# Kernel optimization log

Hardware: AMD Instinct MI355X
Metric: run time of the kernel (lower is better)

The kernel has to match this reference:

```python
import jax, jax.numpy as jnp
import numpy as np

B, S, D, H = 2, 2048, 1024, 16  # batch, seq_len, model dim, heads


def setup_inputs() -> dict:
    key = jax.random.key(0)
    ks = jax.random.split(key, 5)
    return {
        "x": jax.random.normal(ks[0], (B, S, D), jnp.float32),
        "idx": jax.random.randint(ks[1], (B,), 0, S),
        "weight": jnp.float32(0.5),
        "attn_forcing": 1,  # static python flag
        "w_qkv": jax.random.normal(ks[2], (D, 3 * D), jnp.float32) * 0.02,
        "b_qkv": jnp.zeros((3 * D,), jnp.float32),
        "w_proj": jax.random.normal(ks[3], (D, D), jnp.float32) * 0.02,
        "b_proj": jnp.zeros((D,), jnp.float32),
    }


def reference(x, idx, weight, attn_forcing, w_qkv, b_qkv, w_proj, b_proj):
    Bx, Sx, Dm = x.shape
    dh = Dm // H
    # qkv projection (Conv1D: x @ w + b)
    qkv = x @ w_qkv + b_qkv  # [B,S,3D]
    q, k, v = jnp.split(qkv, 3, axis=-1)
    q = q.reshape(Bx, Sx, H, dh).transpose(0, 2, 1, 3)  # [B,H,S,dh]
    k = k.reshape(Bx, Sx, H, dh).transpose(0, 2, 1, 3)
    v = v.reshape(Bx, Sx, H, dh).transpose(0, 2, 1, 3)
    alen = jnp.arange(Sx)
    mask = (alen[None, :] <= alen[:, None]).astype(x.dtype)  # [S,S] causal
    w = jnp.einsum('bhqd,bhkd->bhqk', q, k) / jnp.asarray(np.sqrt(dh), x.dtype)
    w = w * mask + jnp.asarray(-1e9, x.dtype) * (1 - mask)
    w = jax.nn.softmax(w, axis=-1)
    if attn_forcing:
        # post-softmax forcing reweight: positions >= idx scaled by weight, then renorm
        a = jnp.where(alen[None, :] >= idx[:, None], weight, jnp.asarray(1.0, x.dtype))  # [B,S]
        w = w * a[:, None, None, :]
        w = w / jnp.sum(w, axis=-1, keepdims=True)
    out = jnp.einsum('bhqk,bhkd->bhqd', w, v)  # [B,H,S,dh]
    out = out.transpose(0, 2, 1, 3).reshape(Bx, Sx, Dm)  # merge heads
    return out @ w_proj + b_proj
```

## Files before the change

### kernel.cpp

```cpp
#include <hip/hip_runtime.h>


typedef __attribute__((ext_vector_type(8))) short short8;
typedef __attribute__((ext_vector_type(4))) float f32x4;

#define MFMA_B16(a, b, c) __builtin_amdgcn_mfma_f32_16x16x32_bf16(a, b, c, 0, 0, 0)

#if __has_builtin(__builtin_amdgcn_exp2f)
#define EXP2(x) __builtin_amdgcn_exp2f(x)
#else
#define EXP2(x) exp2f(x)
#endif

static __device__ __forceinline__ unsigned short f2bf(float f) {
    union { float f; unsigned int u; } v;
    v.f = f;
    unsigned int r = (v.u + 0x7fffu + ((v.u >> 16) & 1u)) >> 16;
    return (unsigned short)r;
}

static __device__ __forceinline__ unsigned int pk_bf16(float a, float b) {
#if __has_builtin(__builtin_amdgcn_cvt_pk_bf16_f32)
    typedef __bf16 bf2 __attribute__((ext_vector_type(2)));
    union { bf2 v; unsigned int u; } c;
    c.v = __builtin_amdgcn_cvt_pk_bf16_f32(a, b);
    return c.u;
#else
    return (unsigned int)f2bf(a) | ((unsigned int)f2bf(b) << 16);
#endif
}

static __device__ __forceinline__ void gl_lds16(const void* g, void* l) {
    __builtin_amdgcn_global_load_lds(
        (const __attribute__((address_space(1))) unsigned int*)g,
        (__attribute__((address_space(3))) unsigned int*)l, 16, 0, 0);
}

__global__ __launch_bounds__(256) void prep_kernel(const float4* __restrict__ x,
                                                   ushort4* __restrict__ xb,
                                                   const float* __restrict__ wqkv,
                                                   unsigned short* __restrict__ wqkvT,
                                                   const float* __restrict__ wproj,
                                                   unsigned short* __restrict__ wprojT) {
    const int bid = blockIdx.x;
    if (bid < 4096) {
        int i = bid * 256 + threadIdx.x;
        float4 v = x[i];
        ushort4 o;
        o.x = f2bf(v.x); o.y = f2bf(v.y); o.z = f2bf(v.z); o.w = f2bf(v.w);
        xb[i] = o;
        return;
    }
    __shared__ float t[32][33];
    const float* in;
    unsigned short* out;
    int R, C, bx, by;
    if (bid < 4096 + 3072) {
        int g = bid - 4096;
        in = wqkv; out = wqkvT; R = 1024; C = 3072;
        bx = g % 96; by = g / 96;
    } else {
        int g = bid - 7168;
        in = wproj; out = wprojT; R = 1024; C = 1024;
        bx = g & 31; by = g >> 5;
    }
    const int c0 = bx * 32, r0 = by * 32;
    const int xx = threadIdx.x & 31, yy0 = threadIdx.x >> 5;
    #pragma unroll
    for (int yy = yy0; yy < 32; yy += 8)
        t[yy][xx] = in[(size_t)(r0 + yy) * C + (c0 + xx)];
    __syncthreads();
    #pragma unroll
    for (int yy = yy0; yy < 32; yy += 8)
        out[(size_t)(c0 + yy) * R + (r0 + xx)] = f2bf(t[xx][yy]);
}

__global__ __launch_bounds__(256) void gemm_qkv_kernel(const unsigned short* __restrict__ A,
                                                       const unsigned short* __restrict__ Bt,
                                                       const float* __restrict__ bias,
                                                       unsigned short* __restrict__ q,
                                                       unsigned short* __restrict__ k,
                                                       unsigned short* __restrict__ vT) {
    __shared__ unsigned short As[128 * 64];
    __shared__ unsigned short Bs[128 * 64];
    const int tid = threadIdx.x;
    const int lane = tid & 63, wave = tid >> 6;
    const int l15 = lane & 15, quad = lane >> 4;
    const int wm = wave >> 1, wn = wave & 1;
    const int row0 = blockIdx.y * 128, col0 = blockIdx.x * 128;
    const int K = 1024;
    const bool isV = (blockIdx.x >= 16);

    int srow[4], scol[4], sdst[4];
    #pragma unroll
    for (int h = 0; h < 4; ++h) {
        int D = h * 256 + wave * 64 + lane;
        srow[h] = D >> 3;
        scol[h] = ((D & 7) ^ (srow[h] & 7)) * 8;
        sdst[h] = (h * 256 + wave * 64) * 8;
    }

    f32x4 acc[4][4] = {};

    for (int kt = 0; kt < K; kt += 64) {
        #pragma unroll
        for (int h = 0; h < 4; ++h) {
            gl_lds16(&A[(size_t)(row0 + srow[h]) * K + kt + scol[h]], &As[sdst[h]]);
            gl_lds16(&Bt[(size_t)(col0 + srow[h]) * K + kt + scol[h]], &Bs[sdst[h]]);
        }
        __syncthreads();
        #pragma unroll
        for (int kk = 0; kk < 2; ++kk) {
            short8 af[4], bf[4];
            #pragma unroll
            for (int i = 0; i < 4; ++i) {
                int r = wm * 64 + i * 16 + l15;
                af[i] = *(const short8*)&As[r * 64 + (((kk * 4 + quad) ^ (r & 7)) * 8)];
            }
            #pragma unroll
            for (int j = 0; j < 4; ++j) {
                int r = wn * 64 + j * 16 + l15;
                bf[j] = *(const short8*)&Bs[r * 64 + (((kk * 4 + quad) ^ (r & 7)) * 8)];
            }
            if (isV) {
                #pragma unroll
                for (int i = 0; i < 4; ++i)
                    #pragma unroll
                    for (int j = 0; j < 4; ++j)
                        acc[i][j] = MFMA_B16(af[i], bf[j], acc[i][j]);
            } else {
                #pragma unroll
                for (int i = 0; i < 4; ++i)
                    #pragma unroll
                    for (int j = 0; j < 4; ++j)
                        acc[i][j] = MFMA_B16(bf[j], af[i], acc[i][j]);
            }
        }
        __syncthreads();
    }

    const int b = row0 >> 11;
    const int s0 = row0 & 2047;
    const float* bb = bias + col0 + wn * 64;

    if (!isV) {
        const int which = blockIdx.x >> 3;
        unsigned short* dst = which ? k : q;
        const float scale = which ? 1.0f : 0.1803368867f;
        const int hh = ((blockIdx.x & 7) << 1) + wn;
        #pragma unroll
        for (int i = 0; i < 4; ++i) {
            const int s = s0 + wm * 64 + i * 16 + l15;
            unsigned short* drow = dst + ((size_t)((b * 16 + hh) * 2048 + s)) * 64;
            #pragma unroll
            for (int j = 0; j < 4; ++j) {
                float4 b4 = ((const float4*)bb)[j * 4 + quad];
                uint2 pv;
                pv.x = pk_bf16((acc[i][j][0] + b4.x) * scale, (acc[i][j][1] + b4.y) * scale);
                pv.y = pk_bf16((acc[i][j][2] + b4.z) * scale, (acc[i][j][3] + b4.w) * scale);
                *(uint2*)&drow[j * 16 + quad * 4] = pv;
            }
        }
    } else {
        const int hh = ((blockIdx.x - 16) << 1) + wn;
        #pragma unroll
        for (int j = 0; j < 4; ++j) {
            const int d = j * 16 + l15;
            const float bv = bb[d];
            unsigned short* drow = vT + ((size_t)((b * 16 + hh) * 64 + d)) * 2048 + s0;
            #pragma unroll
            for (int i = 0; i < 4; ++i) {
                uint2 pv;
                pv.x = pk_bf16(acc[i][j][0] + bv, acc[i][j][1] + bv);
                pv.y = pk_bf16(acc[i][j][2] + bv, acc[i][j][3] + bv);
                *(uint2*)&drow[wm * 64 + i * 16 + quad * 4] = pv;
            }
        }
    }
}

__global__ __launch_bounds__(256) void gemm_proj_kernel(const unsigned short* __restrict__ A,
                                                        const unsigned short* __restrict__ Bt,
                                                        const float* __restrict__ bias,
                                                        float* __restrict__ out) {
    __shared__ unsigned short As[128 * 64];
    __shared__ unsigned short Bs[64 * 64];
    const int tid = threadIdx.x;
    const int lane = tid & 63, wave = tid >> 6;
    const int l15 = lane & 15, quad = lane >> 4;
    const int wm = wave >> 1, wn = wave & 1;
    const int row0 = blockIdx.y * 128, col0 = blockIdx.x * 64;
    const int K = 1024;

    int srow[4], scol[4], sdst[4];
    #pragma unroll
    for (int h = 0; h < 4; ++h) {
        int D = h * 256 + wave * 64 + lane;
        srow[h] = D >> 3;
        scol[h] = ((D & 7) ^ (srow[h] & 7)) * 8;
        sdst[h] = (h * 256 + wave * 64) * 8;
    }

    f32x4 acc[4][2] = {};

    for (int kt = 0; kt < K; kt += 64) {
        #pragma unroll
        for (int h = 0; h < 4; ++h)
            gl_lds16(&A[(size_t)(row0 + srow[h]) * K + kt + scol[h]], &As[sdst[h]]);
        #pragma unroll
        for (int h = 0; h < 2; ++h)
            gl_lds16(&Bt[(size_t)(col0 + srow[h]) * K + kt + scol[h]], &Bs[sdst[h]]);
        __syncthreads();
        #pragma unroll
        for (int kk = 0; kk < 2; ++kk) {
            short8 af[4], bf[2];
            #pragma unroll
            for (int i = 0; i < 4; ++i) {
                int r = wm * 64 + i * 16 + l15;
                af[i] = *(const short8*)&As[r * 64 + (((kk * 4 + quad) ^ (r & 7)) * 8)];
            }
            #pragma unroll
            for (int j = 0; j < 2; ++j) {
                int r = wn * 32 + j * 16 + l15;
                bf[j] = *(const short8*)&Bs[r * 64 + (((kk * 4 + quad) ^ (r & 7)) * 8)];
            }
            #pragma unroll
            for (int i = 0; i < 4; ++i)
                #pragma unroll
                for (int j = 0; j < 2; ++j)
                    acc[i][j] = MFMA_B16(bf[j], af[i], acc[i][j]);
        }
        __syncthreads();
    }

    const float* bb = bias + col0 + wn * 32;
    #pragma unroll
    for (int i = 0; i < 4; ++i) {
        const int row = row0 + wm * 64 + i * 16 + l15;
        #pragma unroll
        for (int j = 0; j < 2; ++j) {
            float4 b4 = ((const float4*)bb)[j * 4 + quad];
            float4 ov;
            ov.x = acc[i][j][0] + b4.x;
            ov.y = acc[i][j][1] + b4.y;
            ov.z = acc[i][j][2] + b4.z;
            ov.w = acc[i][j][3] + b4.w;
            *(float4*)&out[(size_t)row * 1024 + col0 + wn * 32 + j * 16 + quad * 4] = ov;
        }
    }
}

__global__ __launch_bounds__(256) void attn_kernel(const unsigned short* __restrict__ Q,
                                                   const unsigned short* __restrict__ Kg,
                                                   const unsigned short* __restrict__ Vt,
                                                   const int* __restrict__ idx,
                                                   const float* __restrict__ weight,
                                                   const int* __restrict__ forcing,
                                                   unsigned short* __restrict__ O) {
    __shared__ unsigned short Ks[2][4096];
    __shared__ unsigned short Vs[2][4096];
    __shared__ unsigned short Pw[4][2048];

    const int tid = threadIdx.x;
    const int lane = tid & 63, wave = tid >> 6;
    const int l15 = lane & 15, quad = lane >> 4;
    const int bid = blockIdx.x;
    const int t = 15 - (bid >> 5);
    const int bh = bid & 31;
    const int b = bh >> 4, hh = bh & 15;
    const unsigned short* Qb = Q + (size_t)bh * 2048 * 64;
    const unsigned short* Kh = Kg + (size_t)bh * 2048 * 64;
    const unsigned short* Vh = Vt + (size_t)bh * 2048 * 64;

    const int idxb = idx[b];
    const float lw = (forcing[0] != 0) ? __log2f(weight[0]) : 0.0f;

    const int L0 = wave * 128 + lane;
    const int rS = L0 >> 3;
    const int cS = (L0 & 7) ^ (rS & 7);
    const int ldsOffJ0 = (wave * 128) * 8;
    const int ldsOffJ1 = (wave * 128 + 64) * 8;

    const int q0 = t * 128 + wave * 16;
    const int qrowA = q0 + l15;
    const int qrowB = q0 + 64 + l15;

    short8 aqA0 = *(const short8*)&Qb[(q0 + l15) * 64 + quad * 8];
    short8 aqA1 = *(const short8*)&Qb[(q0 + l15) * 64 + 32 + quad * 8];
    short8 aqB0 = *(const short8*)&Qb[(q0 + 64 + l15) * 64 + quad * 8];
    short8 aqB1 = *(const short8*)&Qb[(q0 + 64 + l15) * 64 + 32 + quad * 8];

    const short8 ones8 = {0x3F80, 0x3F80, 0x3F80, 0x3F80, 0x3F80, 0x3F80, 0x3F80, 0x3F80};

    f32x4 oA[4] = {}, oB[4] = {};
    f32x4 lsA = {}, lsB = {};

    const int nkb = 2 * t + 2;

    {
        const unsigned short* kg = Kh + (size_t)rS * 64 + cS * 8;
        const unsigned short* vg = Vh + (size_t)rS * 2048 + cS * 8;
        gl_lds16(kg,            &Ks[0][ldsOffJ0]);
        gl_lds16(kg + 8 * 64,   &Ks[0][ldsOffJ1]);
        gl_lds16(vg,            &Vs[0][ldsOffJ0]);
        gl_lds16(vg + 8 * 2048, &Vs[0][ldsOffJ1]);
    }
    __syncthreads();

    unsigned short* const pwb = &Pw[wave][0];
    const int pwr = l15 * 64;
    const int pa7 = l15 & 7;

    for (int kb = 0; kb < nkb; ++kb) {
        const int cur = kb & 1;
        const int kbase = kb * 64;
        if (kb + 1 < nkb) {
            const int nb = kbase + 64;
            const unsigned short* kg = Kh + (size_t)(nb + rS) * 64 + cS * 8;
            const unsigned short* vg = Vh + (size_t)rS * 2048 + nb + cS * 8;
            gl_lds16(kg,            &Ks[cur ^ 1][ldsOffJ0]);
            gl_lds16(kg + 8 * 64,   &Ks[cur ^ 1][ldsOffJ1]);
            gl_lds16(vg,            &Vs[cur ^ 1][ldsOffJ0]);
            gl_lds16(vg + 8 * 2048, &Vs[cur ^ 1][ldsOffJ1]);
        }

        const bool liveA = (kb + 1 < nkb);
        const bool diagA = (kb + 2 == nkb);
        const bool diagB = (kb + 1 == nkb);

        const bool fullF = (kbase >= idxb);
        const bool bndF = (!fullF) && (kbase + 63 >= idxb);
        const float zu = fullF ? lw : 0.0f;
        f32x4 zi[4];
        #pragma unroll
        for (int kt = 0; kt < 4; ++kt) {
            if (!bndF) {
                zi[kt][0] = zu; zi[kt][1] = zu; zi[kt][2] = zu; zi[kt][3] = zu;
            } else {
                #pragma unroll
                for (int r = 0; r < 4; ++r)
                    zi[kt][r] = (kbase + kt * 16 + quad * 4 + r >= idxb) ? lw : 0.0f;
            }
        }

        f32x4 sA[4], sB[4];
        #pragma unroll
        for (int kt = 0; kt < 4; ++kt) {
            const int row = kt * 16 + l15;
            short8 k0 = *(const short8*)&Ks[cur][row * 64 + ((quad ^ (row & 7)) * 8)];
            short8 k1 = *(const short8*)&Ks[cur][row * 64 + (((4 + quad) ^ (row & 7)) * 8)];
            if (liveA) {
                f32x4 z = zi[kt];
                z = MFMA_B16(k0, aqA0, z);
                z = MFMA_B16(k1, aqA1, z);
                sA[kt] = z;
            }
            f32x4 z = zi[kt];
            z = MFMA_B16(k0, aqB0, z);
            z = MFMA_B16(k1, aqB1, z);
            sB[kt] = z;
        }

        if (diagA) {
            #pragma unroll
            for (int kt = 0; kt < 4; ++kt)
                #pragma unroll
                for (int r = 0; r < 4; ++r)
                    if (kbase + kt * 16 + quad * 4 + r > qrowA) sA[kt][r] = -3.0e38f;
        }
        if (diagB) {
            #pragma unroll
            for (int kt = 0; kt < 4; ++kt)
                #pragma unroll
                for (int r = 0; r < 4; ++r)
                    if (kbase + kt * 16 + quad * 4 + r > qrowB) sB[kt][r] = -3.0e38f;
        }

        if (liveA) {
            #pragma unroll
            for (int kt = 0; kt < 4; ++kt) {
                #pragma unroll
                for (int r = 0; r < 4; ++r) sA[kt][r] = EXP2(sA[kt][r]);
                unsigned int* pw = (unsigned int*)&pwb[pwr +
                    (((kt * 2 + (quad >> 1)) ^ pa7) * 8) + (quad & 1) * 4];
                pw[0] = pk_bf16(sA[kt][0], sA[kt][1]);
                pw[1] = pk_bf16(sA[kt][2], sA[kt][3]);
            }
        }
        #pragma unroll
        for (int kt = 0; kt < 4; ++kt) {
            #pragma unroll
            for (int r = 0; r < 4; ++r) sB[kt][r] = EXP2(sB[kt][r]);
            unsigned int* pw = (unsigned int*)&pwb[1024 + pwr +
                (((kt * 2 + (quad >> 1)) ^ pa7) * 8) + (quad & 1) * 4];
            pw[0] = pk_bf16(sB[kt][0], sB[kt][1]);
            pw[1] = pk_bf16(sB[kt][2], sB[kt][3]);
        }

        short8 bpA0, bpA1;
        if (liveA) {
            bpA0 = *(const short8*)&pwb[pwr + ((quad ^ pa7) * 8)];
            bpA1 = *(const short8*)&pwb[pwr + (((4 + quad) ^ pa7) * 8)];
            lsA = MFMA_B16(ones8, bpA0, lsA);
            lsA = MFMA_B16(ones8, bpA1, lsA);
        }
        short8 bpB0 = *(const short8*)&pwb[1024 + pwr + ((quad ^ pa7) * 8)];
        short8 bpB1 = *(const short8*)&pwb[1024 + pwr + (((4 + quad) ^ pa7) * 8)];
        lsB = MFMA_B16(ones8, bpB0, lsB);
        lsB = MFMA_B16(ones8, bpB1, lsB);

        #pragma unroll
        for (int dt = 0; dt < 4; ++dt) {
            const int row = dt * 16 + l15;
            short8 vf0 = *(const short8*)&Vs[cur][row * 64 + ((quad ^ (row & 7)) * 8)];
            short8 vf1 = *(const short8*)&Vs[cur][row * 64 + (((4 + quad) ^ (row & 7)) * 8)];
            if (liveA) {
                f32x4 oo = oA[dt];
                oo = MFMA_B16(vf0, bpA0, oo);
                oo = MFMA_B16(vf1, bpA1, oo);
                oA[dt] = oo;
            }
            f32x4 oo = oB[dt];
            oo = MFMA_B16(vf0, bpB0, oo);
            oo = MFMA_B16(vf1, bpB1, oo);
            oB[dt] = oo;
        }

        __syncthreads();
    }

    unsigned short* sc = &Ks[0][0] + wave * 1152;
    {
        const float inv = 1.0f / lsA[0];
        #pragma unroll
        for (int dt = 0; dt < 4; ++dt)
            #pragma unroll
            for (int r = 0; r < 4; ++r)
                sc[l15 * 72 + dt * 16 + quad * 4 + r] = f2bf(oA[dt][r] * inv);
        const size_t rowoff = ((size_t)(b * 2048 + q0 + l15)) * 1024 + hh * 64;
        #pragma unroll
        for (int h = 0; h < 2; ++h) {
            short8 v8 = *(const short8*)&sc[l15 * 72 + quad * 16 + h * 8];
            *(short8*)&O[rowoff + quad * 16 + h * 8] = v8;
        }
    }
    {
        const float inv = 1.0f / lsB[0];
        #pragma unroll
        for (int dt = 0; dt < 4; ++dt)
            #pragma unroll
            for (int r = 0; r < 4; ++r)
                sc[l15 * 72 + dt * 16 + quad * 4 + r] = f2bf(oB[dt][r] * inv);
        const size_t rowoff = ((size_t)(b * 2048 + q0 + 64 + l15)) * 1024 + hh * 64;
        #pragma unroll
        for (int h = 0; h < 2; ++h) {
            short8 v8 = *(const short8*)&sc[l15 * 72 + quad * 16 + h * 8];
            *(short8*)&O[rowoff + quad * 16 + h * 8] = v8;
        }
    }
}

extern "C" void kernel_launch(void* const* d_in, const int* in_sizes, int n_in,
                              void* d_out, int out_size, void* d_ws, size_t ws_size,
                              hipStream_t stream) {
    const float* x        = (const float*)d_in[0];
    const int*   idx      = (const int*)d_in[1];
    const float* weight   = (const float*)d_in[2];
    const int*   forcing  = (const int*)d_in[3];
    const float* w_qkv    = (const float*)d_in[4];
    const float* b_qkv    = (const float*)d_in[5];
    const float* w_proj   = (const float*)d_in[6];
    const float* b_proj   = (const float*)d_in[7];
    float* out = (float*)d_out;

    char* ws = (char*)d_ws;
    unsigned short* xb      = (unsigned short*)(ws);
    unsigned short* wqkvT   = (unsigned short*)(ws + 8388608);
    unsigned short* wprojT  = (unsigned short*)(ws + 14680064);
    unsigned short* qbuf    = (unsigned short*)(ws + 16777216);
    unsigned short* kbuf    = (unsigned short*)(ws + 25165824);
    unsigned short* vTbuf   = (unsigned short*)(ws + 33554432);
    unsigned short* attn_out = xb;

    prep_kernel<<<8192, 256, 0, stream>>>((const float4*)x, (ushort4*)xb,
                                          w_qkv, wqkvT, w_proj, wprojT);
    gemm_qkv_kernel<<<dim3(24, 32), 256, 0, stream>>>(xb, wqkvT, b_qkv, qbuf, kbuf, vTbuf);
    attn_kernel<<<512, 256, 0, stream>>>(qbuf, kbuf, vTbuf, idx, weight, forcing, attn_out);
    gemm_proj_kernel<<<dim3(16, 32), 256, 0, stream>>>(attn_out, wprojT, b_proj, out);
}
```

Before: 209.4 us.

## Split attention into 64-row query tiles with two waves and balanced tile ordering

The attention kernel moves from 128-query-row blocks of four waves to 64-query-row blocks of two waves, launching twice as many blocks. Each wave now owns two adjacent 16-row groups in the same 64-key tile, so every key block is live for both groups and the per-group liveA/diag branching goes away. Block ids are remapped so that long and short causal tiles alternate (31-a, 16+a, 15-a, a) for better load balance across CUs. The cost is that each block re-streams K/V for only half as many query rows, roughly doubling K/V traffic into LDS, and each thread now issues four async loads per operand per tile.

```diff
diff --git a/kernel.cpp b/kernel.cpp
--- a/kernel.cpp
+++ b/kernel.cpp
@@ -250,7 +250,7 @@
     }
 }
 
-__global__ __launch_bounds__(256) void attn_kernel(const unsigned short* __restrict__ Q,
+__global__ __launch_bounds__(128) void attn_kernel(const unsigned short* __restrict__ Q,
                                                    const unsigned short* __restrict__ Kg,
                                                    const unsigned short* __restrict__ Vt,
                                                    const int* __restrict__ idx,
@@ -259,13 +259,14 @@
                                                    unsigned short* __restrict__ O) {
     __shared__ unsigned short Ks[2][4096];
     __shared__ unsigned short Vs[2][4096];
-    __shared__ unsigned short Pw[4][2048];
+    __shared__ unsigned short Pw[2][2048];
 
     const int tid = threadIdx.x;
     const int lane = tid & 63, wave = tid >> 6;
     const int l15 = lane & 15, quad = lane >> 4;
     const int bid = blockIdx.x;
-    const int t = 15 - (bid >> 5);
+    const int u = bid >> 5, a = u & 7, qg = u >> 3;
+    const int t = (qg == 0) ? (31 - a) : (qg == 1) ? (16 + a) : (qg == 2) ? (15 - a) : a;
     const int bh = bid & 31;
     const int b = bh >> 4, hh = bh & 15;
     const unsigned short* Qb = Q + (size_t)bh * 2048 * 64;
@@ -275,35 +276,37 @@
     const int idxb = idx[b];
     const float lw = (forcing[0] != 0) ? __log2f(weight[0]) : 0.0f;
 
-    const int L0 = wave * 128 + lane;
-    const int rS = L0 >> 3;
-    const int cS = (L0 & 7) ^ (rS & 7);
-    const int ldsOffJ0 = (wave * 128) * 8;
-    const int ldsOffJ1 = (wave * 128 + 64) * 8;
-
-    const int q0 = t * 128 + wave * 16;
+    int rS[4], cS[4], dstc[4];
+    #pragma unroll
+    for (int j = 0; j < 4; ++j) {
+        int c = (j * 2 + wave) * 64 + lane;
+        rS[j] = c >> 3;
+        cS[j] = (c & 7) ^ (rS[j] & 7);
+        dstc[j] = ((j * 2 + wave) * 64) * 8;
+    }
+
+    const int q0 = t * 64 + wave * 32;
     const int qrowA = q0 + l15;
-    const int qrowB = q0 + 64 + l15;
+    const int qrowB = q0 + 16 + l15;
 
     short8 aqA0 = *(const short8*)&Qb[(q0 + l15) * 64 + quad * 8];
     short8 aqA1 = *(const short8*)&Qb[(q0 + l15) * 64 + 32 + quad * 8];
-    short8 aqB0 = *(const short8*)&Qb[(q0 + 64 + l15) * 64 + quad * 8];
-    short8 aqB1 = *(const short8*)&Qb[(q0 + 64 + l15) * 64 + 32 + quad * 8];
+    short8 aqB0 = *(const short8*)&Qb[(q0 + 16 + l15) * 64 + quad * 8];
+    short8 aqB1 = *(const short8*)&Qb[(q0 + 16 + l15) * 64 + 32 + quad * 8];
 
     const short8 ones8 = {0x3F80, 0x3F80, 0x3F80, 0x3F80, 0x3F80, 0x3F80, 0x3F80, 0x3F80};
 
     f32x4 oA[4] = {}, oB[4] = {};
     f32x4 lsA = {}, lsB = {};
 
-    const int nkb = 2 * t + 2;
+    const int nkb = t + 1;
 
     {
-        const unsigned short* kg = Kh + (size_t)rS * 64 + cS * 8;
-        const unsigned short* vg = Vh + (size_t)rS * 2048 + cS * 8;
-        gl_lds16(kg,            &Ks[0][ldsOffJ0]);
-        gl_lds16(kg + 8 * 64,   &Ks[0][ldsOffJ1]);
-        gl_lds16(vg,            &Vs[0][ldsOffJ0]);
-        gl_lds16(vg + 8 * 2048, &Vs[0][ldsOffJ1]);
+        #pragma unroll
+        for (int j = 0; j < 4; ++j) {
+            gl_lds16(Kh + (size_t)rS[j] * 64 + cS[j] * 8,   &Ks[0][dstc[j]]);
+            gl_lds16(Vh + (size_t)rS[j] * 2048 + cS[j] * 8, &Vs[0][dstc[j]]);
+        }
     }
     __syncthreads();
 
@@ -316,17 +319,12 @@
         const int kbase = kb * 64;
         if (kb + 1 < nkb) {
             const int nb = kbase + 64;
-            const unsigned short* kg = Kh + (size_t)(nb + rS) * 64 + cS * 8;
-            const unsigned short* vg = Vh + (size_t)rS * 2048 + nb + cS * 8;
-            gl_lds16(kg,            &Ks[cur ^ 1][ldsOffJ0]);
-            gl_lds16(kg + 8 * 64,   &Ks[cur ^ 1][ldsOffJ1]);
-            gl_lds16(vg,            &Vs[cur ^ 1][ldsOffJ0]);
-            gl_lds16(vg + 8 * 2048, &Vs[cur ^ 1][ldsOffJ1]);
-        }
-
-        const bool liveA = (kb + 1 < nkb);
-        const bool diagA = (kb + 2 == nkb);
-        const bool diagB = (kb + 1 == nkb);
+            #pragma unroll
+            for (int j = 0; j < 4; ++j) {
+                gl_lds16(Kh + (size_t)(nb + rS[j]) * 64 + cS[j] * 8,   &Ks[cur ^ 1][dstc[j]]);
+                gl_lds16(Vh + (size_t)rS[j] * 2048 + nb + cS[j] * 8,   &Vs[cur ^ 1][dstc[j]]);
+            }
+        }
 
         const bool fullF = (kbase >= idxb);
         const bool bndF = (!fullF) && (kbase + 63 >= idxb);
@@ -343,40 +341,27 @@
             }
         }
 
-        f32x4 sA[4], sB[4];
-        #pragma unroll
-        for (int kt = 0; kt < 4; ++kt) {
-            const int row = kt * 16 + l15;
-            short8 k0 = *(const short8*)&Ks[cur][row * 64 + ((quad ^ (row & 7)) * 8)];
-            short8 k1 = *(const short8*)&Ks[cur][row * 64 + (((4 + quad) ^ (row & 7)) * 8)];
-            if (liveA) {
+        const bool diag = (kb + 1 == nkb);
+
+        {
+            f32x4 sA[4];
+            #pragma unroll
+            for (int kt = 0; kt < 4; ++kt) {
+                const int row = kt * 16 + l15;
+                short8 k0 = *(const short8*)&Ks[cur][row * 64 + ((quad ^ (row & 7)) * 8)];
+                short8 k1 = *(const short8*)&Ks[cur][row * 64 + (((4 + quad) ^ (row & 7)) * 8)];
                 f32x4 z = zi[kt];
                 z = MFMA_B16(k0, aqA0, z);
                 z = MFMA_B16(k1, aqA1, z);
                 sA[kt] = z;
             }
-            f32x4 z = zi[kt];
-            z = MFMA_B16(k0, aqB0, z);
-            z = MFMA_B16(k1, aqB1, z);
-            sB[kt] = z;
-        }
-
-        if (diagA) {
-            #pragma unroll
-            for (int kt = 0; kt < 4; ++kt)
-                #pragma unroll
-                for (int r = 0; r < 4; ++r)
-                    if (kbase + kt * 16 + quad * 4 + r > qrowA) sA[kt][r] = -3.0e38f;
-        }
-        if (diagB) {
-            #pragma unroll
-            for (int kt = 0; kt < 4; ++kt)
-                #pragma unroll
-                for (int r = 0; r < 4; ++r)
-                    if (kbase + kt * 16 + quad * 4 + r > qrowB) sB[kt][r] = -3.0e38f;
-        }
-
-        if (liveA) {
+            if (diag) {
+                #pragma unroll
+                for (int kt = 0; kt < 4; ++kt)
+                    #pragma unroll
+                    for (int r = 0; r < 4; ++r)
+                        if (kbase + kt * 16 + quad * 4 + r > qrowA) sA[kt][r] = -3.0e38f;
+            }
             #pragma unroll
             for (int kt = 0; kt < 4; ++kt) {
                 #pragma unroll
@@ -387,25 +372,42 @@
                 pw[1] = pk_bf16(sA[kt][2], sA[kt][3]);
             }
         }
-        #pragma unroll
-        for (int kt = 0; kt < 4; ++kt) {
-            #pragma unroll
-            for (int r = 0; r < 4; ++r) sB[kt][r] = EXP2(sB[kt][r]);
-            unsigned int* pw = (unsigned int*)&pwb[1024 + pwr +
-                (((kt * 2 + (quad >> 1)) ^ pa7) * 8) + (quad & 1) * 4];
-            pw[0] = pk_bf16(sB[kt][0], sB[kt][1]);
-            pw[1] = pk_bf16(sB[kt][2], sB[kt][3]);
-        }
-
-        short8 bpA0, bpA1;
-        if (liveA) {
-            bpA0 = *(const short8*)&pwb[pwr + ((quad ^ pa7) * 8)];
-            bpA1 = *(const short8*)&pwb[pwr + (((4 + quad) ^ pa7) * 8)];
-            lsA = MFMA_B16(ones8, bpA0, lsA);
-            lsA = MFMA_B16(ones8, bpA1, lsA);
-        }
+        {
+            f32x4 sB[4];
+            #pragma unroll
+            for (int kt = 0; kt < 4; ++kt) {
+                const int row = kt * 16 + l15;
+                short8 k0 = *(const short8*)&Ks[cur][row * 64 + ((quad ^ (row & 7)) * 8)];
+                short8 k1 = *(const short8*)&Ks[cur][row * 64 + (((4 + quad) ^ (row & 7)) * 8)];
+                f32x4 z = zi[kt];
+                z = MFMA_B16(k0, aqB0, z);
+                z = MFMA_B16(k1, aqB1, z);
+                sB[kt] = z;
+            }
+            if (diag) {
+                #pragma unroll
+                for (int kt = 0; kt < 4; ++kt)
+                    #pragma unroll
+                    for (int r = 0; r < 4; ++r)
+                        if (kbase + kt * 16 + quad * 4 + r > qrowB) sB[kt][r] = -3.0e38f;
+            }
+            #pragma unroll
+            for (int kt = 0; kt < 4; ++kt) {
+                #pragma unroll
+                for (int r = 0; r < 4; ++r) sB[kt][r] = EXP2(sB[kt][r]);
+                unsigned int* pw = (unsigned int*)&pwb[1024 + pwr +
+                    (((kt * 2 + (quad >> 1)) ^ pa7) * 8) + (quad & 1) * 4];
+                pw[0] = pk_bf16(sB[kt][0], sB[kt][1]);
+                pw[1] = pk_bf16(sB[kt][2], sB[kt][3]);
+            }
+        }
+
+        short8 bpA0 = *(const short8*)&pwb[pwr + ((quad ^ pa7) * 8)];
+        short8 bpA1 = *(const short8*)&pwb[pwr + (((4 + quad) ^ pa7) * 8)];
         short8 bpB0 = *(const short8*)&pwb[1024 + pwr + ((quad ^ pa7) * 8)];
         short8 bpB1 = *(const short8*)&pwb[1024 + pwr + (((4 + quad) ^ pa7) * 8)];
+        lsA = MFMA_B16(ones8, bpA0, lsA);
+        lsA = MFMA_B16(ones8, bpA1, lsA);
         lsB = MFMA_B16(ones8, bpB0, lsB);
         lsB = MFMA_B16(ones8, bpB1, lsB);
 
@@ -414,16 +416,14 @@
             const int row = dt * 16 + l15;
             short8 vf0 = *(const short8*)&Vs[cur][row * 64 + ((quad ^ (row & 7)) * 8)];
             short8 vf1 = *(const short8*)&Vs[cur][row * 64 + (((4 + quad) ^ (row & 7)) * 8)];
-            if (liveA) {
-                f32x4 oo = oA[dt];
-                oo = MFMA_B16(vf0, bpA0, oo);
-                oo = MFMA_B16(vf1, bpA1, oo);
-                oA[dt] = oo;
-            }
-            f32x4 oo = oB[dt];
-            oo = MFMA_B16(vf0, bpB0, oo);
-            oo = MFMA_B16(vf1, bpB1, oo);
-            oB[dt] = oo;
+            f32x4 ooA = oA[dt];
+            ooA = MFMA_B16(vf0, bpA0, ooA);
+            ooA = MFMA_B16(vf1, bpA1, ooA);
+            oA[dt] = ooA;
+            f32x4 ooB = oB[dt];
+            ooB = MFMA_B16(vf0, bpB0, ooB);
+            ooB = MFMA_B16(vf1, bpB1, ooB);
+            oB[dt] = ooB;
         }
 
         __syncthreads();
@@ -451,7 +451,7 @@
             #pragma unroll
             for (int r = 0; r < 4; ++r)
                 sc[l15 * 72 + dt * 16 + quad * 4 + r] = f2bf(oB[dt][r] * inv);
-        const size_t rowoff = ((size_t)(b * 2048 + q0 + 64 + l15)) * 1024 + hh * 64;
+        const size_t rowoff = ((size_t)(b * 2048 + q0 + 16 + l15)) * 1024 + hh * 64;
         #pragma unroll
         for (int h = 0; h < 2; ++h) {
             short8 v8 = *(const short8*)&sc[l15 * 72 + quad * 16 + h * 8];
@@ -485,6 +485,6 @@
     prep_kernel<<<8192, 256, 0, stream>>>((const float4*)x, (ushort4*)xb,
                                           w_qkv, wqkvT, w_proj, wprojT);
     gemm_qkv_kernel<<<dim3(24, 32), 256, 0, stream>>>(xb, wqkvT, b_qkv, qbuf, kbuf, vTbuf);
-    attn_kernel<<<512, 256, 0, stream>>>(qbuf, kbuf, vTbuf, idx, weight, forcing, attn_out);
+    attn_kernel<<<1024, 128, 0, stream>>>(qbuf, kbuf, vTbuf, idx, weight, forcing, attn_out);
     gemm_proj_kernel<<<dim3(16, 32), 256, 0, stream>>>(attn_out, wprojT, b_proj, out);
 }
```

Measured after the change: 194.8 us. -7.0%, faster.
